# Kernel tuning notes

Hardware: AMD Instinct MI355X
Metric: run time of the kernel (lower is better)

Reference implementation:

```python
import jax, jax.numpy as jnp
import numpy as np

GS = 128        # grid_size
RES = 0.25      # metres per pixel
CHUNK = 1024    # rows of the pairwise distance matrix materialized at once


def _grid_xy():
    idx = jnp.arange(GS)
    gx, gy = jnp.meshgrid(idx, idx, indexing='ij')  # torch.meshgrid default is 'ij'
    return jnp.stack([gx.ravel() * RES, gy.ravel() * RES], axis=1).astype(jnp.float32)  # [N,2]


def _min_sqdist(a, b):
    """For each point in a [N,3], min squared L2 distance to points in b [N,3].
    Chunked so only a [CHUNK, N] block of the pairwise matrix is live."""
    b2 = jnp.sum(b * b, axis=-1)  # [N]

    def chunk_min(ac):  # ac: [CHUNK,3]
        d = jnp.sum(ac * ac, -1)[:, None] + b2[None, :] - 2.0 * (ac @ b.T)  # [CHUNK,N]
        return jnp.min(jnp.maximum(d, 0.0), axis=-1)

    n = a.shape[0]
    return jax.lax.map(chunk_min, a.reshape(n // CHUNK, CHUNK, 3)).ravel()  # [N]


def reference(inputs, targets):
    xy = _grid_xy()                              # [GS*GS, 2]
    pred_grids = inputs.reshape(-1, GS, GS)      # [G, GS, GS]
    gt_grids = targets.reshape(-1, GS, GS)       # [G, GS, GS]

    def per_grid(args):
        gp, gg = args
        pred = jnp.concatenate([xy, gp.reshape(-1, 1)], axis=1)  # [N,3]
        gt = jnp.concatenate([xy, gg.reshape(-1, 1)], axis=1)    # [N,3]
        # chamfer: dist1 (gt->pred) + dist2 (pred->gt), squared distances
        return jnp.sum(_min_sqdist(gt, pred)) + jnp.sum(_min_sqdist(pred, gt))

    dists = jax.lax.map(per_grid, (pred_grids, gt_grids))  # [G]
    return jnp.mean(dists)


def setup_inputs() -> dict:
    key = jax.random.key(0)
    k1, k2 = jax.random.split(key)
    inputs = jax.random.normal(k1, (1, 1, 512, 512), dtype=jnp.float32)
    targets = jax.random.normal(k2, (1, 512, 512), dtype=jnp.float32)
    return {"inputs": inputs, "targets": targets}
```

## Files before the change

### kernel.cpp

```cpp
#include <hip/hip_runtime.h>

namespace {
constexpr int GS = 128;
constexpr int NPTS = GS * GS;
constexpr float RES = 0.25f;
constexpr int NGRIDS = 16;
constexpr int BLOCK = 256;
constexpr int CHUNKS = NPTS / BLOCK;
constexpr int NBLOCKS = NGRIDS * 2 * CHUNKS;
}

__global__ __launch_bounds__(BLOCK) void chamfer_kernel(
    const float* __restrict__ pred, const float* __restrict__ gt,
    float* __restrict__ partial)
{
    const int bid = blockIdx.x;
    const int chunk = bid & (CHUNKS - 1);
    const int pair = bid >> 6;
    const int g = pair >> 1;
    const int dir = pair & 1;
    const float* __restrict__ A  = (dir == 0) ? gt + g * NPTS : pred + g * NPTS;
    const float* __restrict__ DB = (dir == 0) ? pred + g * NPTS : gt + g * NPTS;

    const int tid = threadIdx.x;
    const int i = chunk * BLOCK + tid;
    const int ri = i >> 7;
    const int ci = i & (GS - 1);
    const float za = A[i];

    int rr[7]; float dx2[7]; int cc[7]; float dy2[7];
    #pragma unroll
    for (int t = 0; t < 7; ++t) {
        int r = min(max(ri + t - 3, 0), GS - 1);
        rr[t] = r;
        const float dx = (float)(ri - r) * RES;
        dx2[t] = dx * dx;
        int c = min(max(ci + t - 3, 0), GS - 1);
        cc[t] = c;
        const float dy = (float)(ci - c) * RES;
        dy2[t] = dy * dy;
    }

    float bacc[4] = {1e30f, 1e30f, 1e30f, 1e30f};
    #pragma unroll
    for (int a = 0; a < 7; ++a) {
        const float* __restrict__ row = DB + rr[a] * GS;
        #pragma unroll
        for (int b = 0; b < 7; ++b) {
            const float z = row[cc[b]];
            const float dz = za - z;
            const int t = a * 7 + b;
            bacc[t & 3] = fminf(bacc[t & 3], fmaf(dz, dz, dx2[a] + dy2[b]));
        }
    }
    float best = fminf(fminf(bacc[0], bacc[1]), fminf(bacc[2], bacc[3]));

    const int lane = tid & 63;
    const int lr = lane >> 3, lc = lane & 7;
    unsigned long long pend = __ballot(best > 1.0f);
    while (pend) {
        const int src = __ffsll(pend) - 1;
        pend &= pend - 1;
        const int qri = __shfl(ri, src);
        const int qci = __shfl(ci, src);
        const float qza = __shfl(za, src);
        const float qb  = __shfl(best, src);
        int K = (int)(4.0f * sqrtf(qb)) + 1;
        K = min(K, GS - 1);
        float m = 1e30f;
        for (int tr = -K; tr <= K; tr += 8) {
            const int dr = tr + lr;
            if (dr > K) continue;
            const int r = min(max(qri + dr, 0), GS - 1);
            const float dx = (float)(qri - r) * RES;
            const float dxx2 = dx * dx;
            const float* __restrict__ row = DB + r * GS;
            for (int tc = -K; tc <= K; tc += 8) {
                const int dc = tc + lc;
                if (dc > K) continue;
                const int c = min(max(qci + dc, 0), GS - 1);
                const float dy = (float)(qci - c) * RES;
                const float dz = qza - row[c];
                m = fminf(m, fmaf(dz, dz, fmaf(dy, dy, dxx2)));
            }
        }
        #pragma unroll
        for (int off = 32; off > 0; off >>= 1) m = fminf(m, __shfl_xor(m, off));
        if (lane == src) best = fminf(best, m);
    }

    for (int off = 32; off > 0; off >>= 1) best += __shfl_down(best, off);
    __shared__ float wsum[BLOCK / 64];
    if ((tid & 63) == 0) wsum[tid >> 6] = best;
    __syncthreads();
    if (tid == 0) {
        float s = 0.0f;
        #pragma unroll
        for (int w = 0; w < BLOCK / 64; ++w) s += wsum[w];
        partial[bid] = s;
    }
}

__global__ __launch_bounds__(1024) void reduce_kernel(
    const float* __restrict__ partial, float* __restrict__ out)
{
    const int tid = threadIdx.x;
    float s = partial[tid] + partial[tid + 1024];
    for (int off = 32; off > 0; off >>= 1) s += __shfl_down(s, off);
    __shared__ float wsum[16];
    if ((tid & 63) == 0) wsum[tid >> 6] = s;
    __syncthreads();
    if (tid == 0) {
        float t = 0.0f;
        #pragma unroll
        for (int w = 0; w < 16; ++w) t += wsum[w];
        *out = t * (1.0f / NGRIDS);
    }
}

extern "C" void kernel_launch(void* const* d_in, const int* in_sizes, int n_in,
                              void* d_out, int out_size, void* d_ws, size_t ws_size,
                              hipStream_t stream) {
    const float* pred = (const float*)d_in[0];
    const float* gt   = (const float*)d_in[1];
    float* partial = (float*)d_ws;
    float* out = (float*)d_out;
    chamfer_kernel<<<NBLOCKS, BLOCK, 0, stream>>>(pred, gt, partial);
    reduce_kernel<<<1, 1024, 0, stream>>>(partial, out);
}
```

Measured before the change: 17.23 us.

## Pad database grids and process four queries per thread with float4 loads

Adds a pre-pass kernel that copies each grid into a 136x136 padded buffer whose border holds a huge sentinel value, so the 7x7 window needs no clamping. Each thread then handles four adjacent query points and loads three float4s per window row, so one set of loads is shared by four queries, and the offset costs become compile-time constants. The grid and the partial-sum count shrink by a factor of four. In exchange the change adds an extra kernel launch and a padded copy written to workspace memory, and thread-level parallelism drops.

```diff
diff --git a/kernel.cpp b/kernel.cpp
--- a/kernel.cpp
+++ b/kernel.cpp
@@ -4,116 +4,155 @@
 constexpr int GS = 128;
 constexpr int NPTS = GS * GS;
 constexpr float RES = 0.25f;
+constexpr float RES2 = RES * RES;
 constexpr int NGRIDS = 16;
+constexpr int PW = 136;
+constexpr int PH = 136;
+constexpr int PADN = PW * PH;
+constexpr float PADV = 1.0e18f;
 constexpr int BLOCK = 256;
-constexpr int CHUNKS = NPTS / BLOCK;
-constexpr int NBLOCKS = NGRIDS * 2 * CHUNKS;
+constexpr int QPT = 4;
+constexpr int TASKS_PER_PAIR = NPTS / QPT;
+constexpr int BLOCKS_PER_PAIR = TASKS_PER_PAIR / BLOCK;
+constexpr int NPAIRS = NGRIDS * 2;
+constexpr int NBLOCKS = NPAIRS * BLOCKS_PER_PAIR;
+constexpr int PAD_QUADS = 2 * NGRIDS * PH * (PW / 4);
+}
+
+__global__ __launch_bounds__(BLOCK) void pad_kernel(
+    const float* __restrict__ pred, const float* __restrict__ gt,
+    float* __restrict__ wpad)
+{
+    const int e4 = blockIdx.x * BLOCK + threadIdx.x;
+    constexpr int QPG = PH * (PW / 4);
+    const int p   = e4 / QPG;
+    const int rem = e4 - p * QPG;
+    const int pr  = rem / (PW / 4);
+    const int c4  = rem - pr * (PW / 4);
+    const int r  = pr - 4;
+    const int c0 = 4 * c4 - 4;
+    float4 v = make_float4(PADV, PADV, PADV, PADV);
+    if (r >= 0 && r < GS && c0 >= 0 && c0 + 3 < GS) {
+        const float* src = (p < NGRIDS) ? pred + p * NPTS : gt + (p - NGRIDS) * NPTS;
+        v = *reinterpret_cast<const float4*>(src + r * GS + c0);
+    }
+    reinterpret_cast<float4*>(wpad)[e4] = v;
 }
 
 __global__ __launch_bounds__(BLOCK) void chamfer_kernel(
     const float* __restrict__ pred, const float* __restrict__ gt,
-    float* __restrict__ partial)
+    const float* __restrict__ wpad, float* __restrict__ partial)
 {
     const int bid = blockIdx.x;
-    const int chunk = bid & (CHUNKS - 1);
-    const int pair = bid >> 6;
+    const int pair = bid >> 4;
+    const int blkin = bid & (BLOCKS_PER_PAIR - 1);
     const int g = pair >> 1;
     const int dir = pair & 1;
-    const float* __restrict__ A  = (dir == 0) ? gt + g * NPTS : pred + g * NPTS;
-    const float* __restrict__ DB = (dir == 0) ? pred + g * NPTS : gt + g * NPTS;
+    const float* __restrict__ A   = (dir == 0) ? gt + g * NPTS : pred + g * NPTS;
+    const float* __restrict__ DBo = (dir == 0) ? pred + g * NPTS : gt + g * NPTS;
+    const float* __restrict__ DBp = wpad + ((dir == 0) ? g : NGRIDS + g) * PADN;
 
     const int tid = threadIdx.x;
-    const int i = chunk * BLOCK + tid;
-    const int ri = i >> 7;
-    const int ci = i & (GS - 1);
-    const float za = A[i];
+    const int task = blkin * BLOCK + tid;
+    const int ri  = task >> 5;
+    const int ci0 = (task & 31) * 4;
 
-    int rr[7]; float dx2[7]; int cc[7]; float dy2[7];
-    #pragma unroll
-    for (int t = 0; t < 7; ++t) {
-        int r = min(max(ri + t - 3, 0), GS - 1);
-        rr[t] = r;
-        const float dx = (float)(ri - r) * RES;
-        dx2[t] = dx * dx;
-        int c = min(max(ci + t - 3, 0), GS - 1);
-        cc[t] = c;
-        const float dy = (float)(ci - c) * RES;
-        dy2[t] = dy * dy;
+    float za[QPT];
+    {
+        const float4 aq = *reinterpret_cast<const float4*>(A + ri * GS + ci0);
+        za[0] = aq.x; za[1] = aq.y; za[2] = aq.z; za[3] = aq.w;
     }
 
-    float bacc[4] = {1e30f, 1e30f, 1e30f, 1e30f};
+    float acc[QPT][2];
     #pragma unroll
-    for (int a = 0; a < 7; ++a) {
-        const float* __restrict__ row = DB + rr[a] * GS;
+    for (int j = 0; j < QPT; ++j) { acc[j][0] = 1e30f; acc[j][1] = 1e30f; }
+
+    #pragma unroll
+    for (int dr = -3; dr <= 3; ++dr) {
+        const float* rp = DBp + (ri + dr + 4) * PW + ci0;
+        const float4 q0 = *reinterpret_cast<const float4*>(rp);
+        const float4 q1 = *reinterpret_cast<const float4*>(rp + 4);
+        const float4 q2 = *reinterpret_cast<const float4*>(rp + 8);
+        const float z[12] = {q0.x, q0.y, q0.z, q0.w,
+                             q1.x, q1.y, q1.z, q1.w,
+                             q2.x, q2.y, q2.z, q2.w};
         #pragma unroll
-        for (int b = 0; b < 7; ++b) {
-            const float z = row[cc[b]];
-            const float dz = za - z;
-            const int t = a * 7 + b;
-            bacc[t & 3] = fminf(bacc[t & 3], fmaf(dz, dz, dx2[a] + dy2[b]));
+        for (int j = 0; j < QPT; ++j) {
+            #pragma unroll
+            for (int dc = -3; dc <= 3; ++dc) {
+                const float dz = za[j] - z[j + dc + 4];
+                const float c2 = (float)(dr * dr + dc * dc) * RES2;
+                acc[j][dc & 1] = fminf(acc[j][dc & 1], fmaf(dz, dz, c2));
+            }
         }
     }
-    float best = fminf(fminf(bacc[0], bacc[1]), fminf(bacc[2], bacc[3]));
+    float best[QPT];
+    #pragma unroll
+    for (int j = 0; j < QPT; ++j) best[j] = fminf(acc[j][0], acc[j][1]);
 
     const int lane = tid & 63;
     const int lr = lane >> 3, lc = lane & 7;
-    unsigned long long pend = __ballot(best > 1.0f);
-    while (pend) {
-        const int src = __ffsll(pend) - 1;
-        pend &= pend - 1;
-        const int qri = __shfl(ri, src);
-        const int qci = __shfl(ci, src);
-        const float qza = __shfl(za, src);
-        const float qb  = __shfl(best, src);
-        int K = (int)(4.0f * sqrtf(qb)) + 1;
-        K = min(K, GS - 1);
-        float m = 1e30f;
-        for (int tr = -K; tr <= K; tr += 8) {
-            const int dr = tr + lr;
-            if (dr > K) continue;
-            const int r = min(max(qri + dr, 0), GS - 1);
-            const float dx = (float)(qri - r) * RES;
-            const float dxx2 = dx * dx;
-            const float* __restrict__ row = DB + r * GS;
-            for (int tc = -K; tc <= K; tc += 8) {
-                const int dc = tc + lc;
-                if (dc > K) continue;
-                const int c = min(max(qci + dc, 0), GS - 1);
-                const float dy = (float)(qci - c) * RES;
-                const float dz = qza - row[c];
-                m = fminf(m, fmaf(dz, dz, fmaf(dy, dy, dxx2)));
+    #pragma unroll
+    for (int j = 0; j < QPT; ++j) {
+        unsigned long long pend = __ballot(best[j] > 1.0f);
+        while (pend) {
+            const int src = __ffsll(pend) - 1;
+            pend &= pend - 1;
+            const int qri = __shfl(ri, src);
+            const int qci = __shfl(ci0, src) + j;
+            const float qza = __shfl(za[j], src);
+            const float qb  = __shfl(best[j], src);
+            int K = (int)(4.0f * sqrtf(qb)) + 1;
+            K = min(K, GS - 1);
+            float m = 1e30f;
+            for (int tr = -K; tr <= K; tr += 8) {
+                const int dr = tr + lr;
+                if (dr > K) continue;
+                const int r = min(max(qri + dr, 0), GS - 1);
+                const float dx = (float)(qri - r) * RES;
+                const float dxx2 = dx * dx;
+                const float* __restrict__ row = DBo + r * GS;
+                for (int tc = -K; tc <= K; tc += 8) {
+                    const int dc = tc + lc;
+                    if (dc > K) continue;
+                    const int c = min(max(qci + dc, 0), GS - 1);
+                    const float dy = (float)(qci - c) * RES;
+                    const float dz = qza - row[c];
+                    m = fminf(m, fmaf(dz, dz, fmaf(dy, dy, dxx2)));
+                }
             }
+            #pragma unroll
+            for (int off = 32; off > 0; off >>= 1) m = fminf(m, __shfl_xor(m, off));
+            if (lane == src) best[j] = fminf(best[j], m);
         }
-        #pragma unroll
-        for (int off = 32; off > 0; off >>= 1) m = fminf(m, __shfl_xor(m, off));
-        if (lane == src) best = fminf(best, m);
     }
 
-    for (int off = 32; off > 0; off >>= 1) best += __shfl_down(best, off);
+    float s = (best[0] + best[1]) + (best[2] + best[3]);
+    for (int off = 32; off > 0; off >>= 1) s += __shfl_down(s, off);
     __shared__ float wsum[BLOCK / 64];
-    if ((tid & 63) == 0) wsum[tid >> 6] = best;
-    __syncthreads();
-    if (tid == 0) {
-        float s = 0.0f;
-        #pragma unroll
-        for (int w = 0; w < BLOCK / 64; ++w) s += wsum[w];
-        partial[bid] = s;
-    }
-}
-
-__global__ __launch_bounds__(1024) void reduce_kernel(
-    const float* __restrict__ partial, float* __restrict__ out)
-{
-    const int tid = threadIdx.x;
-    float s = partial[tid] + partial[tid + 1024];
-    for (int off = 32; off > 0; off >>= 1) s += __shfl_down(s, off);
-    __shared__ float wsum[16];
     if ((tid & 63) == 0) wsum[tid >> 6] = s;
     __syncthreads();
     if (tid == 0) {
         float t = 0.0f;
         #pragma unroll
-        for (int w = 0; w < 16; ++w) t += wsum[w];
+        for (int w = 0; w < BLOCK / 64; ++w) t += wsum[w];
+        partial[bid] = t;
+    }
+}
+
+__global__ __launch_bounds__(512) void reduce_kernel(
+    const float* __restrict__ partial, float* __restrict__ out)
+{
+    const int tid = threadIdx.x;
+    float s = partial[tid];
+    for (int off = 32; off > 0; off >>= 1) s += __shfl_down(s, off);
+    __shared__ float wsum[8];
+    if ((tid & 63) == 0) wsum[tid >> 6] = s;
+    __syncthreads();
+    if (tid == 0) {
+        float t = 0.0f;
+        #pragma unroll
+        for (int w = 0; w < 8; ++w) t += wsum[w];
         *out = t * (1.0f / NGRIDS);
     }
 }
@@ -123,8 +162,10 @@
                               hipStream_t stream) {
     const float* pred = (const float*)d_in[0];
     const float* gt   = (const float*)d_in[1];
-    float* partial = (float*)d_ws;
+    float* wpad    = (float*)d_ws;
+    float* partial = wpad + 2 * NGRIDS * PADN;
     float* out = (float*)d_out;
-    chamfer_kernel<<<NBLOCKS, BLOCK, 0, stream>>>(pred, gt, partial);
-    reduce_kernel<<<1, 1024, 0, stream>>>(partial, out);
+    pad_kernel<<<PAD_QUADS / BLOCK, BLOCK, 0, stream>>>(pred, gt, wpad);
+    chamfer_kernel<<<NBLOCKS, BLOCK, 0, stream>>>(pred, gt, wpad, partial);
+    reduce_kernel<<<1, 512, 0, stream>>>(partial, out);
 }
```

Measured after the change: 23.89 us. 1.39x slower.
